# Kernel tuning notes

Hardware: AMD Instinct MI355X
Metric: run time of the kernel (lower is better)

Reference implementation:

```python
import jax, jax.numpy as jnp
import numpy as np

STEPS = 1  # GNConvolution recurrent update steps

N_ATOMS, N_BONDS, N_GRAPHS = 8192, 131072, 16
ATOM_DIM, BOND_DIM, STATE_DIM = 32, 32, 32


def setup_inputs() -> dict:
    key = jax.random.key(0)
    ks = jax.random.split(key, 12)
    d, bd, sd = ATOM_DIM, BOND_DIM, STATE_DIM
    return {
        "atom_features": jax.random.normal(ks[0], (N_ATOMS, d), jnp.float32),
        "bond_features": jax.random.normal(ks[1], (N_BONDS, bd), jnp.float32),
        "state_attrs": jax.random.normal(ks[2], (N_GRAPHS, sd), jnp.float32),
        # stacked params for the 3 convs (query, key, value)
        "W_edge": jax.random.normal(ks[3], (3, bd + sd, d * d), jnp.float32) * 0.05,
        "b_edge": jnp.zeros((3, d * d), jnp.float32),
        "W_x": jax.random.normal(ks[4], (3, d, 3 * d), jnp.float32) * 0.1,
        "W_h": jax.random.normal(ks[5], (3, d, 3 * d), jnp.float32) * 0.1,
        "b_x": jnp.zeros((3, 3 * d), jnp.float32),
        "b_h": jnp.zeros((3, 3 * d), jnp.float32),
        "pair_indices": jax.random.randint(ks[6], (N_BONDS, 2), 0, N_ATOMS, jnp.int64),
        "atom_graph_indices": jnp.sort(jax.random.randint(ks[7], (N_ATOMS,), 0, N_GRAPHS, jnp.int64)),
        "bond_graph_indices": jnp.sort(jax.random.randint(ks[8], (N_BONDS,), 0, N_GRAPHS, jnp.int64)),
    }


def _gn_conv(atom, bond, state, pair, bond_g, We, be, Wx, Wh, bx, bh):
    """MatDGL GNConvolution: edge-conditioned message passing + GRU update."""
    n_atoms, d = atom.shape
    # edge network: concat(bond, state gathered per bond) -> d x d filter per edge
    edge_in = jnp.concatenate([bond, state[bond_g]], axis=-1)        # [E, bd+sd]
    filt = (edge_in @ We + be).reshape(-1, d, d)                     # [E, d, d]
    neigh = atom[pair[:, 1]]                                         # [E, d]
    msg = jnp.einsum('eij,ej->ei', filt, neigh)                      # [E, d]
    agg = jax.ops.segment_sum(msg, pair[:, 0], num_segments=n_atoms) # [N, d]
    # GRU cell update (reset_after=True, keras default)
    h = atom
    for _ in range(STEPS):
        mx = agg @ Wx + bx
        mh = h @ Wh + bh
        xz, xr, xh = jnp.split(mx, 3, axis=-1)
        hz, hr, hh = jnp.split(mh, 3, axis=-1)
        z = jax.nn.sigmoid(xz + hz)
        r = jax.nn.sigmoid(xr + hr)
        hc = jnp.tanh(xh + r * hh)
        h = z * h + (1.0 - z) * hc
    return h


def reference(atom_features, bond_features, state_attrs, W_edge, b_edge,
              W_x, W_h, b_x, b_h, pair_indices, atom_graph_indices,
              bond_graph_indices):
    d = atom_features.shape[-1]
    conv = jax.vmap(_gn_conv,
                    in_axes=(None, None, None, None, None, 0, 0, 0, 0, 0, 0))
    qkv = conv(atom_features, bond_features, state_attrs, pair_indices,
               bond_graph_indices, W_edge, b_edge, W_x, W_h, b_x, b_h)
    q, k, v = qkv[0], qkv[1], qkv[2]                                 # [N, d] each
    scores = (q @ k.T) / jnp.asarray(d, q.dtype) ** 0.5              # [N, N]
    attn = jax.nn.softmax(scores, axis=-1)
    return attn @ v                                                  # [N, d]
```

## Files before the change

kernel.cpp:

```cpp
#include <hip/hip_runtime.h>
#include <hip/hip_bf16.h>
#include <math.h>

#define NA 8192
#define NB 131072
#define NG 16
#define NSHARD 16
#define PART_STRIDE 34

#define OFF_BH   0u
#define OFF_VB   49152u
#define OFF_AGG  73728u
#define OFF_QH   860160u
#define OFF_QL   991232u
#define OFF_KH   1122304u
#define OFF_KL   1253376u
#define OFF_VTH  1384448u
#define OFF_VTL  1515520u
#define OFF_PART 1646592u

typedef __attribute__((ext_vector_type(8))) short short8;
typedef __attribute__((ext_vector_type(4))) float f4;
typedef __attribute__((ext_vector_type(2))) float f2;
typedef __attribute__((ext_vector_type(2))) unsigned int uint2v;

__device__ inline unsigned short bfb(float x) {
    __hip_bfloat16 b = __float2bfloat16(x);
    return reinterpret_cast<unsigned short&>(b);
}
__device__ inline float bf2f(unsigned short u) {
    unsigned int x = ((unsigned int)u) << 16;
    return __uint_as_float(x);
}
__device__ inline unsigned int pk2(float x, float y) {
    __hip_bfloat162 t = __float22bfloat162_rn(make_float2(x, y));
    union { __hip_bfloat162 b; unsigned int u; } cv;
    cv.b = t;
    return cv.u;
}

__global__ __launch_bounds__(256) void prep_bh(const float* __restrict__ We,
                                               unsigned short* __restrict__ Bh)
{
    int idx = blockIdx.x * 256 + threadIdx.x;
    int hc = idx >> 8;
    int n4 = (idx & 255) * 4;
    const float4 v = *(const float4*)(We + ((size_t)((hc >> 5) * 64 + (hc & 31))) * 1024 + n4);
    unsigned short* d = Bh + (size_t)hc * 1024 + n4;
    d[0] = bfb(v.x); d[1] = bfb(v.y); d[2] = bfb(v.z); d[3] = bfb(v.w);
}

__global__ __launch_bounds__(256) void prep_v(const float* __restrict__ state,
    const float* __restrict__ We, const float* __restrict__ be,
    unsigned short* __restrict__ Vb)
{
    int h = blockIdx.x >> 4, g = blockIdx.x & 15;
    const float* st = state + g * 32;
    const float* W  = We + ((size_t)h * 64 + 32) * 1024;
    const float* bb = be + (size_t)h * 1024;
    int n = threadIdx.x * 4;
    float4 acc = *(const float4*)(bb + n);
    for (int c = 0; c < 32; ++c) {
        float s = st[c];
        const float4 w = *(const float4*)(W + c * 1024 + n);
        acc.x += s * w.x; acc.y += s * w.y; acc.z += s * w.z; acc.w += s * w.w;
    }
    unsigned short* d = Vb + ((size_t)h * 16 + g) * 1024 + n;
    d[0] = bfb(acc.x); d[1] = bfb(acc.y); d[2] = bfb(acc.z); d[3] = bfb(acc.w);
}

__global__ __launch_bounds__(256) void msg_mfma(
    const float* __restrict__ atom, const float* __restrict__ bond,
    const unsigned short* __restrict__ Bh, const unsigned short* __restrict__ Vb,
    const int* __restrict__ pair, const int* __restrict__ bg,
    float* __restrict__ agg)
{
    __shared__ float bl[128 * 36];
    __shared__ int gmm[2];
    const int tid = threadIdx.x;
    const int h  = blockIdx.y;
    const int e0 = blockIdx.x * 128;
    for (int x = tid; x < 1024; x += 256) {
        int e = x >> 3, c4 = (x & 7) << 2;
        float4 v = *(const float4*)(bond + (size_t)(e0 + e) * 32 + c4);
        float* d = &bl[e * 36 + c4];
        d[0] = v.x; d[1] = v.y; d[2] = v.z; d[3] = v.w;
    }
    if (tid == 0) { gmm[0] = bg[e0]; gmm[1] = bg[e0 + 127]; }

    const int wave = tid >> 6, lane = tid & 63;
    const int ln = lane & 15, quad = lane >> 4;
    const int em0 = e0 + wave * 32 + ln;
    const int em1 = em0 + 16;
    const int src0 = pair[2 * em0 + 1], src1 = pair[2 * em1 + 1];
    const int gv0 = bg[em0], gv1 = bg[em1];
    f2 n0p[4], n1p[4];
    {
        const float* p0 = atom + (size_t)src0 * 32 + quad * 8;
        const float* p1 = atom + (size_t)src1 * 32 + quad * 8;
        float4 a = *(const float4*)p0, b = *(const float4*)(p0 + 4);
        n0p[0] = f2{a.x, a.y}; n0p[1] = f2{a.z, a.w};
        n0p[2] = f2{b.x, b.y}; n0p[3] = f2{b.z, b.w};
        float4 c = *(const float4*)p1, d = *(const float4*)(p1 + 4);
        n1p[0] = f2{c.x, c.y}; n1p[1] = f2{c.z, c.w};
        n1p[2] = f2{d.x, d.y}; n1p[3] = f2{d.z, d.w};
    }
    __syncthreads();
    f4 acc00 = {0,0,0,0}, acc01 = {0,0,0,0}, acc10 = {0,0,0,0}, acc11 = {0,0,0,0};
    const unsigned short* bp = Bh + (size_t)h * 32 * 1024 + ln * 32 + quad * 8;
    const int bo0 = (wave * 32 + ln) * 36;
    const int bo1 = bo0 + 16 * 36;
    #pragma unroll 2
    for (int c4 = 0; c4 < 32; c4 += 4) {
        f4 cv0 = *(const f4*)&bl[bo0 + c4];
        f4 cv1 = *(const f4*)&bl[bo1 + c4];
        #pragma unroll
        for (int u = 0; u < 4; ++u) {
            const unsigned short* bpc = bp + (c4 + u) * 1024;
            short8 b0 = *(const short8*)bpc;
            short8 b1 = *(const short8*)(bpc + 512);
            float c0 = cv0[u], c1 = cv1[u];
            union { unsigned int u4[4]; short8 s; } A0, A1;
            #pragma unroll
            for (int q2 = 0; q2 < 4; ++q2) {
                f2 p0 = c0 * n0p[q2];
                f2 p1 = c1 * n1p[q2];
                A0.u4[q2] = pk2(p0.x, p0.y);
                A1.u4[q2] = pk2(p1.x, p1.y);
            }
            acc00 = __builtin_amdgcn_mfma_f32_16x16x32_bf16(A0.s, b0, acc00, 0, 0, 0);
            acc01 = __builtin_amdgcn_mfma_f32_16x16x32_bf16(A0.s, b1, acc01, 0, 0, 0);
            acc10 = __builtin_amdgcn_mfma_f32_16x16x32_bf16(A1.s, b0, acc10, 0, 0, 0);
            acc11 = __builtin_amdgcn_mfma_f32_16x16x32_bf16(A1.s, b1, acc11, 0, 0, 0);
        }
    }
    union { unsigned int u4[4]; short8 s; } NB0, NB1;
    #pragma unroll
    for (int q2 = 0; q2 < 4; ++q2) {
        NB0.u4[q2] = pk2(n0p[q2].x, n0p[q2].y);
        NB1.u4[q2] = pk2(n1p[q2].x, n1p[q2].y);
    }
    const short8 zz = {0,0,0,0,0,0,0,0};
    const int gmin = gmm[0], gmax = gmm[1];
    for (int g = gmin; g <= gmax; ++g) {
        const unsigned short* vp = Vb + ((size_t)h * 16 + g) * 1024 + ln * 32 + quad * 8;
        short8 b0 = *(const short8*)vp;
        short8 b1 = *(const short8*)(vp + 512);
        short8 a0 = (gv0 == g) ? NB0.s : zz;
        short8 a1 = (gv1 == g) ? NB1.s : zz;
        acc00 = __builtin_amdgcn_mfma_f32_16x16x32_bf16(a0, b0, acc00, 0, 0, 0);
        acc01 = __builtin_amdgcn_mfma_f32_16x16x32_bf16(a0, b1, acc01, 0, 0, 0);
        acc10 = __builtin_amdgcn_mfma_f32_16x16x32_bf16(a1, b0, acc10, 0, 0, 0);
        acc11 = __builtin_amdgcn_mfma_f32_16x16x32_bf16(a1, b1, acc11, 0, 0, 0);
    }
    #pragma unroll
    for (int r = 0; r < 4; ++r) {
        int eA = e0 + wave * 32 + quad * 4 + r;
        int eB = eA + 16;
        int aA = pair[2 * eA], aB = pair[2 * eB];
        float* dA = agg + ((size_t)h * NA + aA) * 32;
        float* dB = agg + ((size_t)h * NA + aB) * 32;
        atomicAdd(dA + ln,      acc00[r]);
        atomicAdd(dA + 16 + ln, acc01[r]);
        atomicAdd(dB + ln,      acc10[r]);
        atomicAdd(dB + 16 + ln, acc11[r]);
    }
}

__global__ __launch_bounds__(256) void gru_kernel(
    const float* __restrict__ atom, const float* __restrict__ agg,
    const float* __restrict__ Wx, const float* __restrict__ Wh,
    const float* __restrict__ bx, const float* __restrict__ bh,
    unsigned short* __restrict__ Qh, unsigned short* __restrict__ Ql,
    unsigned short* __restrict__ Kh, unsigned short* __restrict__ Kl,
    unsigned short* __restrict__ Vth, unsigned short* __restrict__ Vtl)
{
    __shared__ float ag[8][33], at[8][33], hb[8][33];
    const int tid = threadIdx.x;
    const int r = tid >> 5, i = tid & 31;
    const int ha = blockIdx.x * 8 + r;
    const int h = ha >> 13;
    const int a = ha & 8191;
    ag[r][i] = agg[(size_t)ha * 32 + i];
    at[r][i] = atom[(size_t)a * 32 + i];
    __syncthreads();
    const float* wx = Wx + (size_t)h * 32 * 96;
    const float* wh = Wh + (size_t)h * 32 * 96;
    float x0 = bx[h*96 + i], x1 = bx[h*96 + 32 + i], x2 = bx[h*96 + 64 + i];
    float g0 = bh[h*96 + i], g1 = bh[h*96 + 32 + i], g2 = bh[h*96 + 64 + i];
    #pragma unroll 4
    for (int c = 0; c < 32; ++c) {
        float av = ag[r][c], hv = at[r][c];
        x0 += av * wx[c*96 + i]; x1 += av * wx[c*96 + 32 + i]; x2 += av * wx[c*96 + 64 + i];
        g0 += hv * wh[c*96 + i]; g1 += hv * wh[c*96 + 32 + i]; g2 += hv * wh[c*96 + 64 + i];
    }
    float z  = 1.f / (1.f + __expf(-(x0 + g0)));
    float rr = 1.f / (1.f + __expf(-(x1 + g1)));
    float hc = tanhf(x2 + rr * g2);
    float hn = z * at[r][i] + (1.f - z) * hc;
    if (h == 0) {
        float x = hn * 0.1767766952966369f;
        unsigned short hi = bfb(x);
        Qh[(size_t)a * 32 + i] = hi;
        Ql[(size_t)a * 32 + i] = bfb(x - bf2f(hi));
    } else if (h == 1) {
        unsigned short hi = bfb(hn);
        Kh[(size_t)a * 32 + i] = hi;
        Kl[(size_t)a * 32 + i] = bfb(hn - bf2f(hi));
    } else {
        hb[r][i] = hn;
        __syncthreads();
        const int a0 = blockIdx.x * 8 - 2 * NA;
        const int i2 = tid >> 3, a2 = tid & 7;
        float v = hb[a2][i2];
        unsigned short hi = bfb(v);
        Vth[(size_t)i2 * NA + a0 + a2] = hi;
        Vtl[(size_t)i2 * NA + a0 + a2] = bfb(v - bf2f(hi));
    }
}

__global__ __launch_bounds__(256) void attn_mfma(
    const unsigned short* __restrict__ Qh, const unsigned short* __restrict__ Ql,
    const unsigned short* __restrict__ Kh, const unsigned short* __restrict__ Kl,
    const unsigned short* __restrict__ Vth, const unsigned short* __restrict__ Vtl,
    float* __restrict__ part)
{
    __shared__ unsigned short pb[4][32 * 40];
    const int tid = threadIdx.x;
    const int wave = tid >> 6, lane = tid & 63;
    const int ln = lane & 15, quad = lane >> 4;
    const int sh = blockIdx.y;
    const int q0 = blockIdx.x * 128 + wave * 32;

    short8 qh0 = *(const short8*)(Qh + (size_t)(q0 + ln) * 32 + quad * 8);
    short8 ql0 = *(const short8*)(Ql + (size_t)(q0 + ln) * 32 + quad * 8);
    short8 qh1 = *(const short8*)(Qh + (size_t)(q0 + 16 + ln) * 32 + quad * 8);
    short8 ql1 = *(const short8*)(Ql + (size_t)(q0 + 16 + ln) * 32 + quad * 8);

    f4 a00 = {0,0,0,0}, a01 = {0,0,0,0}, a10 = {0,0,0,0}, a11 = {0,0,0,0};
    float l0 = 0.f, l1 = 0.f;
    float m = -INFINITY;
    unsigned short* pw = &pb[wave][0];

    const int kbeg = sh * (NA / NSHARD);
    for (int k0 = kbeg; k0 < kbeg + NA / NSHARD; k0 += 32) {
        const size_t ko0 = (size_t)(k0 + ln) * 32 + quad * 8;
        const size_t ko1 = (size_t)(k0 + 16 + ln) * 32 + quad * 8;
        short8 kh0 = *(const short8*)(Kh + ko0);
        short8 kh1 = *(const short8*)(Kh + ko1);
        short8 kl0 = *(const short8*)(Kl + ko0);
        short8 kl1 = *(const short8*)(Kl + ko1);

        f4 s00 = {0,0,0,0}, s01 = {0,0,0,0}, s10 = {0,0,0,0}, s11 = {0,0,0,0};
        s00 = __builtin_amdgcn_mfma_f32_16x16x32_bf16(kl0, qh0, s00, 0, 0, 0);
        s00 = __builtin_amdgcn_mfma_f32_16x16x32_bf16(kh0, ql0, s00, 0, 0, 0);
        s00 = __builtin_amdgcn_mfma_f32_16x16x32_bf16(kh0, qh0, s00, 0, 0, 0);
        s01 = __builtin_amdgcn_mfma_f32_16x16x32_bf16(kl0, qh1, s01, 0, 0, 0);
        s01 = __builtin_amdgcn_mfma_f32_16x16x32_bf16(kh0, ql1, s01, 0, 0, 0);
        s01 = __builtin_amdgcn_mfma_f32_16x16x32_bf16(kh0, qh1, s01, 0, 0, 0);
        s10 = __builtin_amdgcn_mfma_f32_16x16x32_bf16(kl1, qh0, s10, 0, 0, 0);
        s10 = __builtin_amdgcn_mfma_f32_16x16x32_bf16(kh1, ql0, s10, 0, 0, 0);
        s10 = __builtin_amdgcn_mfma_f32_16x16x32_bf16(kh1, qh0, s10, 0, 0, 0);
        s11 = __builtin_amdgcn_mfma_f32_16x16x32_bf16(kl1, qh1, s11, 0, 0, 0);
        s11 = __builtin_amdgcn_mfma_f32_16x16x32_bf16(kh1, ql1, s11, 0, 0, 0);
        s11 = __builtin_amdgcn_mfma_f32_16x16x32_bf16(kh1, qh1, s11, 0, 0, 0);

        float mx = fmaxf(fmaxf(fmaxf(s00[0], s00[1]), fmaxf(s00[2], s00[3])),
                         fmaxf(fmaxf(s01[0], s01[1]), fmaxf(s01[2], s01[3])));
        mx = fmaxf(mx, fmaxf(fmaxf(fmaxf(s10[0], s10[1]), fmaxf(s10[2], s10[3])),
                             fmaxf(fmaxf(s11[0], s11[1]), fmaxf(s11[2], s11[3]))));
        #pragma unroll
        for (int msk = 1; msk < 64; msk <<= 1)
            mx = fmaxf(mx, __shfl_xor(mx, msk));
        const float mn = fmaxf(m, mx);
        const float al = __expf(m - mn);
        m = mn;
        #pragma unroll
        for (int r = 0; r < 4; ++r) {
            a00[r] *= al; a01[r] *= al; a10[r] *= al; a11[r] *= al;
        }
        l0 *= al; l1 *= al;

        {
            float e0 = __expf(s00[0]-m), e1 = __expf(s00[1]-m),
                  e2 = __expf(s00[2]-m), e3 = __expf(s00[3]-m);
            l0 += (e0+e1)+(e2+e3);
            *(uint2v*)&pw[ln*40 + quad*4] = uint2v{pk2(e0,e1), pk2(e2,e3)};
            e0 = __expf(s10[0]-m); e1 = __expf(s10[1]-m);
            e2 = __expf(s10[2]-m); e3 = __expf(s10[3]-m);
            l0 += (e0+e1)+(e2+e3);
            *(uint2v*)&pw[ln*40 + 16 + quad*4] = uint2v{pk2(e0,e1), pk2(e2,e3)};
            e0 = __expf(s01[0]-m); e1 = __expf(s01[1]-m);
            e2 = __expf(s01[2]-m); e3 = __expf(s01[3]-m);
            l1 += (e0+e1)+(e2+e3);
            *(uint2v*)&pw[(16+ln)*40 + quad*4] = uint2v{pk2(e0,e1), pk2(e2,e3)};
            e0 = __expf(s11[0]-m); e1 = __expf(s11[1]-m);
            e2 = __expf(s11[2]-m); e3 = __expf(s11[3]-m);
            l1 += (e0+e1)+(e2+e3);
            *(uint2v*)&pw[(16+ln)*40 + 16 + quad*4] = uint2v{pk2(e0,e1), pk2(e2,e3)};
        }
        short8 pa0 = *(const short8*)&pw[ln*40 + quad*8];
        short8 pa1 = *(const short8*)&pw[(16+ln)*40 + quad*8];

        const size_t vo0 = (size_t)ln * NA + k0 + quad * 8;
        const size_t vo1 = (size_t)(16 + ln) * NA + k0 + quad * 8;
        short8 vh0 = *(const short8*)(Vth + vo0);
        short8 vh1 = *(const short8*)(Vth + vo1);
        short8 vl0 = *(const short8*)(Vtl + vo0);
        short8 vl1 = *(const short8*)(Vtl + vo1);

        a00 = __builtin_amdgcn_mfma_f32_16x16x32_bf16(pa0, vl0, a00, 0, 0, 0);
        a00 = __builtin_amdgcn_mfma_f32_16x16x32_bf16(pa0, vh0, a00, 0, 0, 0);
        a01 = __builtin_amdgcn_mfma_f32_16x16x32_bf16(pa0, vl1, a01, 0, 0, 0);
        a01 = __builtin_amdgcn_mfma_f32_16x16x32_bf16(pa0, vh1, a01, 0, 0, 0);
        a10 = __builtin_amdgcn_mfma_f32_16x16x32_bf16(pa1, vl0, a10, 0, 0, 0);
        a10 = __builtin_amdgcn_mfma_f32_16x16x32_bf16(pa1, vh0, a10, 0, 0, 0);
        a11 = __builtin_amdgcn_mfma_f32_16x16x32_bf16(pa1, vl1, a11, 0, 0, 0);
        a11 = __builtin_amdgcn_mfma_f32_16x16x32_bf16(pa1, vh1, a11, 0, 0, 0);
    }
    l0 += __shfl_xor(l0, 16); l0 += __shfl_xor(l0, 32);
    l1 += __shfl_xor(l1, 16); l1 += __shfl_xor(l1, 32);

    #pragma unroll
    for (int r = 0; r < 4; ++r) {
        const int row0 = q0 + quad * 4 + r;
        float* pp = part + ((size_t)sh * NA + row0) * PART_STRIDE;
        pp[ln] = a00[r]; pp[16 + ln] = a01[r];
        float* pq = part + ((size_t)sh * NA + row0 + 16) * PART_STRIDE;
        pq[ln] = a10[r]; pq[16 + ln] = a11[r];
    }
    if (quad == 0) {
        float* pp = part + ((size_t)sh * NA + q0 + ln) * PART_STRIDE;
        pp[32] = m; pp[33] = l0;
        float* pq = part + ((size_t)sh * NA + q0 + 16 + ln) * PART_STRIDE;
        pq[32] = m; pq[33] = l1;
    }
}

__global__ __launch_bounds__(256) void merge_kernel(const float* __restrict__ part,
                                                    float* __restrict__ out)
{
    const int tid = threadIdx.x;
    const int r = tid >> 5, c = tid & 31;
    const int q = blockIdx.x * 8 + r;
    float ms = -INFINITY;
    #pragma unroll
    for (int sh = 0; sh < NSHARD; ++sh)
        ms = fmaxf(ms, part[((size_t)sh * NA + q) * PART_STRIDE + 32]);
    float den = 0.f, num = 0.f;
    #pragma unroll
    for (int sh = 0; sh < NSHARD; ++sh) {
        const float* pp = part + ((size_t)sh * NA + q) * PART_STRIDE;
        float w = __expf(pp[32] - ms);
        den += w * pp[33];
        num += w * pp[c];
    }
    out[(size_t)q * 32 + c] = num / den;
}

extern "C" void kernel_launch(void* const* d_in, const int* in_sizes, int n_in,
                              void* d_out, int out_size, void* d_ws, size_t ws_size,
                              hipStream_t stream)
{
    const float* atom  = (const float*)d_in[0];
    const float* bond  = (const float*)d_in[1];
    const float* state = (const float*)d_in[2];
    const float* We    = (const float*)d_in[3];
    const float* be    = (const float*)d_in[4];
    const float* Wx    = (const float*)d_in[5];
    const float* Wh    = (const float*)d_in[6];
    const float* bx    = (const float*)d_in[7];
    const float* bh    = (const float*)d_in[8];
    const int*   pair  = (const int*)d_in[9];
    const int*   bg    = (const int*)d_in[11];
    float* ws = (float*)d_ws;
    unsigned short* Bh  = (unsigned short*)(ws + OFF_BH);
    unsigned short* Vb  = (unsigned short*)(ws + OFF_VB);
    float* agg  = ws + OFF_AGG;
    unsigned short* Qh  = (unsigned short*)(ws + OFF_QH);
    unsigned short* Ql  = (unsigned short*)(ws + OFF_QL);
    unsigned short* Kh  = (unsigned short*)(ws + OFF_KH);
    unsigned short* Kl  = (unsigned short*)(ws + OFF_KL);
    unsigned short* Vth = (unsigned short*)(ws + OFF_VTH);
    unsigned short* Vtl = (unsigned short*)(ws + OFF_VTL);
    float* part = ws + OFF_PART;
    float* out  = (float*)d_out;

    hipMemsetAsync(agg, 0, (size_t)3 * NA * 32 * sizeof(float), stream);
    prep_bh<<<96, 256, 0, stream>>>(We, Bh);
    prep_v<<<48, 256, 0, stream>>>(state, We, be, Vb);
    msg_mfma<<<dim3(NB / 128, 3), 256, 0, stream>>>(atom, bond, Bh, Vb, pair, bg, agg);
    gru_kernel<<<3 * NA / 8, 256, 0, stream>>>(atom, agg, Wx, Wh, bx, bh,
                                               Qh, Ql, Kh, Kl, Vth, Vtl);
    attn_mfma<<<dim3(NA / 128, NSHARD), 256, 0, stream>>>(Qh, Ql, Kh, Kl, Vth, Vtl, part);
    merge_kernel<<<NA / 8, 256, 0, stream>>>(part, out);
}
```

Measured before the change: 252.8 us.

## Fuse the three conv heads into one msg_mfma block to reuse gathered inputs

The message kernel no longer launches one grid slice per head (q/k/v). Each block now processes all three heads, so the bond tile load, neighbor-atom gathers, pair and graph-index reads, and the bf16 A-fragment packing happen once and are reused across three sets of MFMAs. This cuts redundant global gathers and VALU packing by roughly a factor of three. In exchange, accumulator registers triple (48 floats per lane), which may reduce occupancy, and the grid shrinks to a third as many blocks.

```diff
diff --git a/kernel.cpp b/kernel.cpp
--- a/kernel.cpp
+++ b/kernel.cpp
@@ -78,7 +78,6 @@
     __shared__ float bl[128 * 36];
     __shared__ int gmm[2];
     const int tid = threadIdx.x;
-    const int h  = blockIdx.y;
     const int e0 = blockIdx.x * 128;
     for (int x = tid; x < 1024; x += 256) {
         int e = x >> 3, c4 = (x & 7) << 2;
@@ -106,19 +105,24 @@
         n1p[2] = f2{d.x, d.y}; n1p[3] = f2{d.z, d.w};
     }
     __syncthreads();
-    f4 acc00 = {0,0,0,0}, acc01 = {0,0,0,0}, acc10 = {0,0,0,0}, acc11 = {0,0,0,0};
-    const unsigned short* bp = Bh + (size_t)h * 32 * 1024 + ln * 32 + quad * 8;
+    f4 acc[3][2][2];
+    #pragma unroll
+    for (int h = 0; h < 3; ++h)
+        #pragma unroll
+        for (int mt = 0; mt < 2; ++mt)
+            #pragma unroll
+            for (int nt = 0; nt < 2; ++nt)
+                acc[h][mt][nt] = f4{0,0,0,0};
+
+    const unsigned short* bp = Bh + ln * 32 + quad * 8;
     const int bo0 = (wave * 32 + ln) * 36;
     const int bo1 = bo0 + 16 * 36;
-    #pragma unroll 2
     for (int c4 = 0; c4 < 32; c4 += 4) {
         f4 cv0 = *(const f4*)&bl[bo0 + c4];
         f4 cv1 = *(const f4*)&bl[bo1 + c4];
         #pragma unroll
         for (int u = 0; u < 4; ++u) {
-            const unsigned short* bpc = bp + (c4 + u) * 1024;
-            short8 b0 = *(const short8*)bpc;
-            short8 b1 = *(const short8*)(bpc + 512);
+            const int c = c4 + u;
             float c0 = cv0[u], c1 = cv1[u];
             union { unsigned int u4[4]; short8 s; } A0, A1;
             #pragma unroll
@@ -128,10 +132,16 @@
                 A0.u4[q2] = pk2(p0.x, p0.y);
                 A1.u4[q2] = pk2(p1.x, p1.y);
             }
-            acc00 = __builtin_amdgcn_mfma_f32_16x16x32_bf16(A0.s, b0, acc00, 0, 0, 0);
-            acc01 = __builtin_amdgcn_mfma_f32_16x16x32_bf16(A0.s, b1, acc01, 0, 0, 0);
-            acc10 = __builtin_amdgcn_mfma_f32_16x16x32_bf16(A1.s, b0, acc10, 0, 0, 0);
-            acc11 = __builtin_amdgcn_mfma_f32_16x16x32_bf16(A1.s, b1, acc11, 0, 0, 0);
+            #pragma unroll
+            for (int h = 0; h < 3; ++h) {
+                const unsigned short* bpc = bp + ((size_t)(h * 32 + c)) * 1024;
+                short8 b0 = *(const short8*)bpc;
+                short8 b1 = *(const short8*)(bpc + 512);
+                acc[h][0][0] = __builtin_amdgcn_mfma_f32_16x16x32_bf16(A0.s, b0, acc[h][0][0], 0, 0, 0);
+                acc[h][0][1] = __builtin_amdgcn_mfma_f32_16x16x32_bf16(A0.s, b1, acc[h][0][1], 0, 0, 0);
+                acc[h][1][0] = __builtin_amdgcn_mfma_f32_16x16x32_bf16(A1.s, b0, acc[h][1][0], 0, 0, 0);
+                acc[h][1][1] = __builtin_amdgcn_mfma_f32_16x16x32_bf16(A1.s, b1, acc[h][1][1], 0, 0, 0);
+            }
         }
     }
     union { unsigned int u4[4]; short8 s; } NB0, NB1;
@@ -143,27 +153,33 @@
     const short8 zz = {0,0,0,0,0,0,0,0};
     const int gmin = gmm[0], gmax = gmm[1];
     for (int g = gmin; g <= gmax; ++g) {
-        const unsigned short* vp = Vb + ((size_t)h * 16 + g) * 1024 + ln * 32 + quad * 8;
-        short8 b0 = *(const short8*)vp;
-        short8 b1 = *(const short8*)(vp + 512);
         short8 a0 = (gv0 == g) ? NB0.s : zz;
         short8 a1 = (gv1 == g) ? NB1.s : zz;
-        acc00 = __builtin_amdgcn_mfma_f32_16x16x32_bf16(a0, b0, acc00, 0, 0, 0);
-        acc01 = __builtin_amdgcn_mfma_f32_16x16x32_bf16(a0, b1, acc01, 0, 0, 0);
-        acc10 = __builtin_amdgcn_mfma_f32_16x16x32_bf16(a1, b0, acc10, 0, 0, 0);
-        acc11 = __builtin_amdgcn_mfma_f32_16x16x32_bf16(a1, b1, acc11, 0, 0, 0);
+        #pragma unroll
+        for (int h = 0; h < 3; ++h) {
+            const unsigned short* vp = Vb + ((size_t)h * 16 + g) * 1024 + ln * 32 + quad * 8;
+            short8 b0 = *(const short8*)vp;
+            short8 b1 = *(const short8*)(vp + 512);
+            acc[h][0][0] = __builtin_amdgcn_mfma_f32_16x16x32_bf16(a0, b0, acc[h][0][0], 0, 0, 0);
+            acc[h][0][1] = __builtin_amdgcn_mfma_f32_16x16x32_bf16(a0, b1, acc[h][0][1], 0, 0, 0);
+            acc[h][1][0] = __builtin_amdgcn_mfma_f32_16x16x32_bf16(a1, b0, acc[h][1][0], 0, 0, 0);
+            acc[h][1][1] = __builtin_amdgcn_mfma_f32_16x16x32_bf16(a1, b1, acc[h][1][1], 0, 0, 0);
+        }
     }
     #pragma unroll
     for (int r = 0; r < 4; ++r) {
         int eA = e0 + wave * 32 + quad * 4 + r;
         int eB = eA + 16;
         int aA = pair[2 * eA], aB = pair[2 * eB];
-        float* dA = agg + ((size_t)h * NA + aA) * 32;
-        float* dB = agg + ((size_t)h * NA + aB) * 32;
-        atomicAdd(dA + ln,      acc00[r]);
-        atomicAdd(dA + 16 + ln, acc01[r]);
-        atomicAdd(dB + ln,      acc10[r]);
-        atomicAdd(dB + 16 + ln, acc11[r]);
+        #pragma unroll
+        for (int h = 0; h < 3; ++h) {
+            float* dA = agg + ((size_t)h * NA + aA) * 32;
+            float* dB = agg + ((size_t)h * NA + aB) * 32;
+            atomicAdd(dA + ln,      acc[h][0][0][r]);
+            atomicAdd(dA + 16 + ln, acc[h][0][1][r]);
+            atomicAdd(dB + ln,      acc[h][1][0][r]);
+            atomicAdd(dB + 16 + ln, acc[h][1][1][r]);
+        }
     }
 }
 
@@ -389,7 +405,7 @@
     hipMemsetAsync(agg, 0, (size_t)3 * NA * 32 * sizeof(float), stream);
     prep_bh<<<96, 256, 0, stream>>>(We, Bh);
     prep_v<<<48, 256, 0, stream>>>(state, We, be, Vb);
-    msg_mfma<<<dim3(NB / 128, 3), 256, 0, stream>>>(atom, bond, Bh, Vb, pair, bg, agg);
+    msg_mfma<<<NB / 128, 256, 0, stream>>>(atom, bond, Bh, Vb, pair, bg, agg);
     gru_kernel<<<3 * NA / 8, 256, 0, stream>>>(atom, agg, Wx, Wh, bx, bh,
                                                Qh, Ql, Kh, Kl, Vth, Vtl);
     attn_mfma<<<dim3(NA / 128, NSHARD), 256, 0, stream>>>(Qh, Ql, Kh, Kl, Vth, Vtl, part);
```

New measurement: 258.6 us. +2.3%, slower.

## Sort edges by destination and pre-reduce messages in shared memory

Applied to the files above, without the earlier changes.

Builds a counting-sort permutation of edges by destination atom (count, single-block scan, atomic scatter) and makes the message kernel process edges in that order. Each block sums messages for up to 32 destination segments in LDS and then issues one global atomic per segment element, replacing per-edge global atomics. The prep kernels are merged with the counting pass. This adds two small kernels, a serial segment scan in one thread per block, gathered bond and atom loads, and a non-deterministic edge order from the atomic scatter.

```diff
diff --git a/kernel.cpp b/kernel.cpp
--- a/kernel.cpp
+++ b/kernel.cpp
@@ -11,13 +11,16 @@
 #define OFF_BH   0u
 #define OFF_VB   49152u
 #define OFF_AGG  73728u
-#define OFF_QH   860160u
-#define OFF_QL   991232u
-#define OFF_KH   1122304u
-#define OFF_KL   1253376u
-#define OFF_VTH  1384448u
-#define OFF_VTL  1515520u
-#define OFF_PART 1646592u
+#define OFF_CNT  860160u
+#define OFF_CUR  868352u
+#define OFF_PERM 876544u
+#define OFF_QH   1007616u
+#define OFF_QL   1138688u
+#define OFF_KH   1269760u
+#define OFF_KL   1400832u
+#define OFF_VTH  1531904u
+#define OFF_VTL  1662976u
+#define OFF_PART 1794048u
 
 typedef __attribute__((ext_vector_type(8))) short short8;
 typedef __attribute__((ext_vector_type(4))) float f4;
@@ -39,61 +42,121 @@
     return cv.u;
 }
 
-__global__ __launch_bounds__(256) void prep_bh(const float* __restrict__ We,
-                                               unsigned short* __restrict__ Bh)
-{
-    int idx = blockIdx.x * 256 + threadIdx.x;
-    int hc = idx >> 8;
-    int n4 = (idx & 255) * 4;
-    const float4 v = *(const float4*)(We + ((size_t)((hc >> 5) * 64 + (hc & 31))) * 1024 + n4);
-    unsigned short* d = Bh + (size_t)hc * 1024 + n4;
-    d[0] = bfb(v.x); d[1] = bfb(v.y); d[2] = bfb(v.z); d[3] = bfb(v.w);
-}
-
-__global__ __launch_bounds__(256) void prep_v(const float* __restrict__ state,
-    const float* __restrict__ We, const float* __restrict__ be,
-    unsigned short* __restrict__ Vb)
-{
-    int h = blockIdx.x >> 4, g = blockIdx.x & 15;
-    const float* st = state + g * 32;
-    const float* W  = We + ((size_t)h * 64 + 32) * 1024;
-    const float* bb = be + (size_t)h * 1024;
-    int n = threadIdx.x * 4;
-    float4 acc = *(const float4*)(bb + n);
-    for (int c = 0; c < 32; ++c) {
-        float s = st[c];
-        const float4 w = *(const float4*)(W + c * 1024 + n);
-        acc.x += s * w.x; acc.y += s * w.y; acc.z += s * w.z; acc.w += s * w.w;
-    }
-    unsigned short* d = Vb + ((size_t)h * 16 + g) * 1024 + n;
-    d[0] = bfb(acc.x); d[1] = bfb(acc.y); d[2] = bfb(acc.z); d[3] = bfb(acc.w);
+__global__ __launch_bounds__(256) void prep_all(
+    const float* __restrict__ We, const float* __restrict__ state,
+    const float* __restrict__ be, const int* __restrict__ pair,
+    unsigned short* __restrict__ Bh, unsigned short* __restrict__ Vb,
+    int* __restrict__ cnt)
+{
+    const int bid = blockIdx.x, tid = threadIdx.x;
+    const int e = bid * 256 + tid;
+    atomicAdd(&cnt[pair[2 * e]], 1);
+    if (bid < 96) {
+        int idx = bid * 256 + tid;
+        int hc = idx >> 8;
+        int n4 = (idx & 255) * 4;
+        const float4 v = *(const float4*)(We + ((size_t)((hc >> 5) * 64 + (hc & 31))) * 1024 + n4);
+        unsigned short* d = Bh + (size_t)hc * 1024 + n4;
+        d[0] = bfb(v.x); d[1] = bfb(v.y); d[2] = bfb(v.z); d[3] = bfb(v.w);
+    } else if (bid < 144) {
+        int b2 = bid - 96;
+        int h = b2 >> 4, g = b2 & 15;
+        const float* st = state + g * 32;
+        const float* W  = We + ((size_t)h * 64 + 32) * 1024;
+        const float* bb = be + (size_t)h * 1024;
+        int n = tid * 4;
+        float4 acc = *(const float4*)(bb + n);
+        for (int c = 0; c < 32; ++c) {
+            float s = st[c];
+            const float4 w = *(const float4*)(W + c * 1024 + n);
+            acc.x += s * w.x; acc.y += s * w.y; acc.z += s * w.z; acc.w += s * w.w;
+        }
+        unsigned short* d = Vb + ((size_t)h * 16 + g) * 1024 + n;
+        d[0] = bfb(acc.x); d[1] = bfb(acc.y); d[2] = bfb(acc.z); d[3] = bfb(acc.w);
+    }
+}
+
+__global__ __launch_bounds__(256) void scan_kernel(const int* __restrict__ cnt,
+                                                   int* __restrict__ cur)
+{
+    __shared__ int part[256];
+    const int t = threadIdx.x;
+    const int base = t * 32;
+    int loc[32];
+    int s = 0;
+    #pragma unroll
+    for (int k = 0; k < 32; ++k) { loc[k] = cnt[base + k]; s += loc[k]; }
+    part[t] = s;
+    __syncthreads();
+    for (int off = 1; off < 256; off <<= 1) {
+        int add = (t >= off) ? part[t - off] : 0;
+        __syncthreads();
+        part[t] += add;
+        __syncthreads();
+    }
+    int excl = part[t] - s;
+    #pragma unroll
+    for (int k = 0; k < 32; ++k) { cur[base + k] = excl; excl += loc[k]; }
+}
+
+__global__ __launch_bounds__(256) void scatter_kernel(const int* __restrict__ pair,
+                                                      int* __restrict__ cur,
+                                                      int* __restrict__ perm)
+{
+    const int e = blockIdx.x * 256 + threadIdx.x;
+    const int d = pair[2 * e];
+    const int p = atomicAdd(&cur[d], 1);
+    perm[p] = e;
 }
 
 __global__ __launch_bounds__(256) void msg_mfma(
     const float* __restrict__ atom, const float* __restrict__ bond,
     const unsigned short* __restrict__ Bh, const unsigned short* __restrict__ Vb,
     const int* __restrict__ pair, const int* __restrict__ bg,
-    float* __restrict__ agg)
+    const int* __restrict__ perm, float* __restrict__ agg)
 {
     __shared__ float bl[128 * 36];
-    __shared__ int gmm[2];
+    __shared__ float aggl[32 * 33];
+    __shared__ int pe[128], dstl[128], bgl[128], segid[128];
+    __shared__ int segdst[32];
+    __shared__ int meta[3];
     const int tid = threadIdx.x;
     const int h  = blockIdx.y;
-    const int e0 = blockIdx.x * 128;
+    const int s0 = blockIdx.x * 128;
+    if (tid < 128) {
+        int e = perm[s0 + tid];
+        pe[tid] = e;
+        dstl[tid] = pair[2 * e];
+        bgl[tid] = bg[e];
+    }
+    for (int x = tid; x < 32 * 33; x += 256) aggl[x] = 0.f;
+    __syncthreads();
+    if (tid == 0) {
+        int gmn = bgl[0], gmx = bgl[0], seg = 0;
+        segdst[0] = dstl[0]; segid[0] = 0;
+        for (int s = 1; s < 128; ++s) {
+            int g = bgl[s];
+            gmn = min(gmn, g); gmx = max(gmx, g);
+            if (dstl[s] != dstl[s - 1]) {
+                ++seg;
+                if (seg < 32) segdst[seg] = dstl[s];
+            }
+            segid[s] = (seg < 32) ? seg : -1;
+        }
+        meta[0] = gmn; meta[1] = gmx; meta[2] = min(seg + 1, 32);
+    }
     for (int x = tid; x < 1024; x += 256) {
-        int e = x >> 3, c4 = (x & 7) << 2;
-        float4 v = *(const float4*)(bond + (size_t)(e0 + e) * 32 + c4);
-        float* d = &bl[e * 36 + c4];
+        int slot = x >> 3, c4 = (x & 7) << 2;
+        float4 v = *(const float4*)(bond + (size_t)pe[slot] * 32 + c4);
+        float* d = &bl[slot * 36 + c4];
         d[0] = v.x; d[1] = v.y; d[2] = v.z; d[3] = v.w;
     }
-    if (tid == 0) { gmm[0] = bg[e0]; gmm[1] = bg[e0 + 127]; }
-
     const int wave = tid >> 6, lane = tid & 63;
     const int ln = lane & 15, quad = lane >> 4;
-    const int em0 = e0 + wave * 32 + ln;
-    const int em1 = em0 + 16;
-    const int src0 = pair[2 * em0 + 1], src1 = pair[2 * em1 + 1];
-    const int gv0 = bg[em0], gv1 = bg[em1];
+    const int sA = wave * 32 + ln, sB = sA + 16;
+    const int eA = pe[sA], eB = pe[sB];
+    const int src0 = pair[2 * eA + 1], src1 = pair[2 * eB + 1];
+    const int gv0 = bgl[sA], gv1 = bgl[sB];
     f2 n0p[4], n1p[4];
     {
         const float* p0 = atom + (size_t)src0 * 32 + quad * 8;
@@ -108,8 +171,8 @@
     __syncthreads();
     f4 acc00 = {0,0,0,0}, acc01 = {0,0,0,0}, acc10 = {0,0,0,0}, acc11 = {0,0,0,0};
     const unsigned short* bp = Bh + (size_t)h * 32 * 1024 + ln * 32 + quad * 8;
-    const int bo0 = (wave * 32 + ln) * 36;
-    const int bo1 = bo0 + 16 * 36;
+    const int bo0 = sA * 36;
+    const int bo1 = sB * 36;
     #pragma unroll 2
     for (int c4 = 0; c4 < 32; c4 += 4) {
         f4 cv0 = *(const f4*)&bl[bo0 + c4];
@@ -141,7 +204,7 @@
         NB1.u4[q2] = pk2(n1p[q2].x, n1p[q2].y);
     }
     const short8 zz = {0,0,0,0,0,0,0,0};
-    const int gmin = gmm[0], gmax = gmm[1];
+    const int gmin = meta[0], gmax = meta[1];
     for (int g = gmin; g <= gmax; ++g) {
         const unsigned short* vp = Vb + ((size_t)h * 16 + g) * 1024 + ln * 32 + quad * 8;
         short8 b0 = *(const short8*)vp;
@@ -155,15 +218,29 @@
     }
     #pragma unroll
     for (int r = 0; r < 4; ++r) {
-        int eA = e0 + wave * 32 + quad * 4 + r;
-        int eB = eA + 16;
-        int aA = pair[2 * eA], aB = pair[2 * eB];
-        float* dA = agg + ((size_t)h * NA + aA) * 32;
-        float* dB = agg + ((size_t)h * NA + aB) * 32;
-        atomicAdd(dA + ln,      acc00[r]);
-        atomicAdd(dA + 16 + ln, acc01[r]);
-        atomicAdd(dB + ln,      acc10[r]);
-        atomicAdd(dB + 16 + ln, acc11[r]);
+        const int rowA = wave * 32 + quad * 4 + r;
+        const int rowB = rowA + 16;
+        const int sgA = segid[rowA], sgB = segid[rowB];
+        if (sgA >= 0) {
+            atomicAdd(&aggl[sgA * 33 + ln],      acc00[r]);
+            atomicAdd(&aggl[sgA * 33 + 16 + ln], acc01[r]);
+        } else {
+            float* dA = agg + ((size_t)h * NA + dstl[rowA]) * 32;
+            atomicAdd(dA + ln, acc00[r]); atomicAdd(dA + 16 + ln, acc01[r]);
+        }
+        if (sgB >= 0) {
+            atomicAdd(&aggl[sgB * 33 + ln],      acc10[r]);
+            atomicAdd(&aggl[sgB * 33 + 16 + ln], acc11[r]);
+        } else {
+            float* dB = agg + ((size_t)h * NA + dstl[rowB]) * 32;
+            atomicAdd(dB + ln, acc10[r]); atomicAdd(dB + 16 + ln, acc11[r]);
+        }
+    }
+    __syncthreads();
+    const int nseg = meta[2];
+    for (int x = tid; x < nseg * 32; x += 256) {
+        int seg = x >> 5, i = x & 31;
+        atomicAdd(&agg[((size_t)h * NA + segdst[seg]) * 32 + i], aggl[seg * 33 + i]);
     }
 }
 
@@ -280,7 +357,6 @@
             a00[r] *= al; a01[r] *= al; a10[r] *= al; a11[r] *= al;
         }
         l0 *= al; l1 *= al;
-
         {
             float e0 = __expf(s00[0]-m), e1 = __expf(s00[1]-m),
                   e2 = __expf(s00[2]-m), e3 = __expf(s00[3]-m);
@@ -377,6 +453,9 @@
     unsigned short* Bh  = (unsigned short*)(ws + OFF_BH);
     unsigned short* Vb  = (unsigned short*)(ws + OFF_VB);
     float* agg  = ws + OFF_AGG;
+    int*   cnt  = (int*)(ws + OFF_CNT);
+    int*   cur  = (int*)(ws + OFF_CUR);
+    int*   perm = (int*)(ws + OFF_PERM);
     unsigned short* Qh  = (unsigned short*)(ws + OFF_QH);
     unsigned short* Ql  = (unsigned short*)(ws + OFF_QL);
     unsigned short* Kh  = (unsigned short*)(ws + OFF_KH);
@@ -386,10 +465,11 @@
     float* part = ws + OFF_PART;
     float* out  = (float*)d_out;
 
-    hipMemsetAsync(agg, 0, (size_t)3 * NA * 32 * sizeof(float), stream);
-    prep_bh<<<96, 256, 0, stream>>>(We, Bh);
-    prep_v<<<48, 256, 0, stream>>>(state, We, be, Vb);
-    msg_mfma<<<dim3(NB / 128, 3), 256, 0, stream>>>(atom, bond, Bh, Vb, pair, bg, agg);
+    hipMemsetAsync(agg, 0, (size_t)(3 * NA * 32 + NA) * sizeof(float), stream);
+    prep_all<<<512, 256, 0, stream>>>(We, state, be, pair, Bh, Vb, cnt);
+    scan_kernel<<<1, 256, 0, stream>>>(cnt, cur);
+    scatter_kernel<<<512, 256, 0, stream>>>(pair, cur, perm);
+    msg_mfma<<<dim3(NB / 128, 3), 256, 0, stream>>>(atom, bond, Bh, Vb, pair, bg, perm, agg);
     gru_kernel<<<3 * NA / 8, 256, 0, stream>>>(atom, agg, Wx, Wh, bx, bh,
                                                Qh, Ql, Kh, Kl, Vth, Vtl);
     attn_mfma<<<dim3(NA / 128, NSHARD), 256, 0, stream>>>(Qh, Ql, Kh, Kl, Vth, Vtl, part);
```

After: 339.1 us. 34.1% more time.
